# Optimization experiments

Measured on AMD Instinct MI355X. Metric: run time of the kernel, lower is better.

Reference implementation:

```python
import jax, jax.numpy as jnp
import numpy as np
from jax import lax

EPS = 1e-5
SLOPE = 0.01  # default leaky_relu negative slope

def _conv1d(x, w):
    # x: [B, Cin, L], w: [Cout, Cin, K]; padding=1 (same for K=3)
    return lax.conv_general_dilated(x, w, window_strides=(1,), padding=[(1, 1)],
                                    dimension_numbers=('NCH', 'OIH', 'NCH'))

def _bn_train(x, gamma, beta, axes):
    # training-mode BatchNorm: batch stats over `axes`, biased variance
    mean = jnp.mean(x, axis=axes, keepdims=True)
    var = jnp.mean(jnp.square(x - mean), axis=axes, keepdims=True)
    shape = [1] * x.ndim
    shape[1] = x.shape[1]
    g = gamma.reshape(shape); b = beta.reshape(shape)
    return (x - mean) * g / jnp.sqrt(var + EPS) + b

def setup_inputs() -> dict:
    key = jax.random.key(0)
    ks = jax.random.split(key, 6)
    d, d2, out_dim = 64, 128, 128
    bs, T, N = 16, 32, 256
    s = 0.05
    return {
        'x': jax.random.normal(ks[0], (bs, T, N, d), jnp.float32),
        'conv1_w': jax.random.normal(ks[1], (d2, d, 3), jnp.float32) * s,
        'bn1_g': jnp.ones((d2,), jnp.float32), 'bn1_b': jnp.zeros((d2,), jnp.float32),
        'conv2_w': jax.random.normal(ks[2], (d2, d2, 3), jnp.float32) * s,
        'bn2_g': jnp.ones((d2,), jnp.float32), 'bn2_b': jnp.zeros((d2,), jnp.float32),
        'map_w': jax.random.normal(ks[3], (d2, d2), jnp.float32) * s,
        'map_b': jnp.zeros((d2,), jnp.float32),
        'theta_w': jax.random.normal(ks[4], (out_dim, d2), jnp.float32) * s,
        'theta_b': jnp.zeros((out_dim,), jnp.float32),
        'bnS_g': jnp.ones((out_dim,), jnp.float32), 'bnS_b': jnp.zeros((out_dim,), jnp.float32),
    }

def reference(x, conv1_w, bn1_g, bn1_b, conv2_w, bn2_g, bn2_b,
              map_w, map_b, theta_w, theta_b, bnS_g, bnS_b):
    bs, T, N, d = x.shape
    d2 = 2 * d
    # ---- Temporal 1D CNN over time, per node ----
    tem = jnp.transpose(x, (0, 2, 1, 3)).reshape(bs * N, T, d)      # [BN, T, d]
    h = jnp.transpose(tem, (0, 2, 1))                               # [BN, d, T]
    h = jax.nn.relu(_bn_train(_conv1d(h, conv1_w), bn1_g, bn1_b, (0, 2)))
    h = jax.nn.relu(_bn_train(_conv1d(h, conv2_w), bn2_g, bn2_b, (0, 2)))  # [BN, 2d, T]
    # faithful raw reshape (mixes channel/time layout exactly like the torch code)
    tem_out = h.reshape(bs, N, T, d2)
    spa = jnp.transpose(tem_out, (0, 2, 1, 3)).reshape(bs * T, N, d2)  # [B', N, 2d]
    # ---- Dot-product graph construction ----
    mapped = jnp.einsum('bnd,ed->bne', spa, map_w) + map_b            # Linear(2d,2d)
    adj = jnp.einsum('bnd,bmd->bnm', mapped, mapped)                  # [B', N, N]
    eye = jnp.eye(N, dtype=adj.dtype)
    adj = jax.nn.leaky_relu(adj - eye * 1e8, SLOPE)
    adj = jax.nn.softmax(adj, axis=-1) + eye
    # ---- MPNN (k=1): theta(A @ X), BN over channels, leaky_relu ----
    agg = jnp.einsum('bnm,bmd->bnd', adj, spa)                        # bmm(A, X)
    out = jnp.einsum('bnd,od->bno', agg, theta_w) + theta_b           # [B', N, out]
    out = jnp.transpose(out, (0, 2, 1))                               # [B', out, N]
    out = _bn_train(out, bnS_g, bnS_b, (0, 2))
    out = jnp.transpose(out, (0, 2, 1))
    return jax.nn.leaky_relu(out, SLOPE)
```

## Files before the change

kernel.cpp:

```cpp
#include <hip/hip_runtime.h>

#define SLOPE 0.01f
#define EPSB 1e-5f
#define INV_CNT (1.0f/131072.0f)

typedef unsigned short u16;
typedef unsigned int u32;
typedef __attribute__((ext_vector_type(8))) short s16x8;
typedef __attribute__((ext_vector_type(4))) float f4;

__device__ float g_stats[3][2][128];
__device__ float g_sb[3][2][128];
__device__ float g_part[2048][256];
__device__ u16 g_w1h[3][128][64];
__device__ u16 g_w1l[3][128][64];
__device__ u16 g_w2h[3][128][128];
__device__ u16 g_w2l[3][128][128];
__device__ u16 g_wmh[128][128];
__device__ u16 g_wml[128][128];
__device__ u16 g_wqh[128][128];
__device__ u16 g_wql[128][128];

__device__ __forceinline__ float lrelu(float x){ return x > 0.f ? x : SLOPE*x; }
__device__ __forceinline__ u16 f2b(float f){
  u32 u = __float_as_uint(f);
  return (u16)((u + 0x7fffu + ((u >> 16) & 1u)) >> 16);
}
__device__ __forceinline__ float b2f(u16 h){ return __uint_as_float(((u32)h) << 16); }
__device__ __forceinline__ u32 pk(float a, float b){ return (u32)f2b(a) | ((u32)f2b(b) << 16); }
__device__ __forceinline__ u32 pkhl(float f){
  u16 h = f2b(f);
  u16 l = f2b(f - b2f(h));
  return (u32)h | ((u32)l << 16);
}
__device__ __forceinline__ float unhl(u32 v){ return b2f((u16)(v & 0xffff)) + b2f((u16)(v >> 16)); }

__global__ void k_zero(){
  int i = blockIdx.x*256 + threadIdx.x;
  if (i < 768) ((float*)g_stats)[i] = 0.f;
}

__global__ void k_reduce(int which){
  const float* base = &g_part[blockIdx.x*128][0];
  int j = threadIdx.x;
  float s = 0.f;
  #pragma unroll 4
  for (int r = 0; r < 128; ++r) s += base[r*256 + j];
  atomicAdd(&((float*)g_stats)[which*256 + j], s);
}

__global__ void k_prepw(const float* __restrict__ w1, const float* __restrict__ w2,
                        const float* __restrict__ mapw, const float* __restrict__ thw){
  int idx = blockIdx.x*256 + threadIdx.x;
  if (idx < 24576){
    int kk = idx >> 13, r = idx & 8191, co = r >> 6, ci = r & 63;
    float v = w1[co*192 + ci*3 + kk];
    u16 h = f2b(v);
    g_w1h[kk][co][ci] = h; g_w1l[kk][co][ci] = f2b(v - b2f(h));
  } else if (idx < 73728){
    int j = idx - 24576;
    int kk = j >> 14, r = j & 16383, co = r >> 7, ci = r & 127;
    float v = w2[co*384 + ci*3 + kk];
    u16 h = f2b(v);
    g_w2h[kk][co][ci] = h; g_w2l[kk][co][ci] = f2b(v - b2f(h));
  } else if (idx < 90112){
    int j = idx - 73728;
    float v = mapw[j];
    u16 h = f2b(v);
    ((u16*)g_wmh)[j] = h; ((u16*)g_wml)[j] = f2b(v - b2f(h));
  } else if (idx < 106496){
    int j = idx - 90112;
    float v = thw[j];
    u16 h = f2b(v);
    ((u16*)g_wqh)[j] = h; ((u16*)g_wql)[j] = f2b(v - b2f(h));
  }
}

__global__ void k_finalize(const float* __restrict__ g, const float* __restrict__ bta, int which){
  int c = threadIdx.x;
  float mean = g_stats[which][0][c] * INV_CNT;
  float var  = g_stats[which][1][c] * INV_CNT - mean*mean;
  float sc = g[c] * rsqrtf(var + EPSB);
  g_sb[which][0][c] = sc;
  g_sb[which][1][c] = bta[c] - mean*sc;
}

__global__ __launch_bounds__(256) void k_conv1(const float* __restrict__ x, u16* __restrict__ y1hl){
  __shared__ __align__(16) u16 a0h[2][34][72];
  __shared__ __align__(16) u16 a0l[2][34][72];
  __shared__ __align__(16) u16 w1s[128][72];
  const int bid = blockIdx.x;
  const int bn0 = bid*2;
  const int b = bn0 >> 8, n = bn0 & 255;
  const int tid = threadIdx.x;
  const int w = tid >> 6, l = tid & 63, quad = l >> 4, lm = l & 15;
  f4 acc[2][4];
  #pragma unroll
  for (int i = 0; i < 2; ++i)
    #pragma unroll
    for (int j = 0; j < 4; ++j) acc[i][j] = (f4)0.f;

  {
    int nn = tid >> 7, rem = tid & 127, t = rem >> 2, ci0 = (rem & 3)*16;
    const float* px = x + ((b*32 + t)*256 + n + nn)*64 + ci0;
    u16 hh[16], ll[16];
    #pragma unroll
    for (int j = 0; j < 4; ++j){
      float4 v = *(const float4*)(px + 4*j);
      float vv[4] = {v.x, v.y, v.z, v.w};
      #pragma unroll
      for (int e = 0; e < 4; ++e){
        u16 h = f2b(vv[e]);
        hh[4*j+e] = h; ll[4*j+e] = f2b(vv[e] - b2f(h));
      }
    }
    *(uint4*)&a0h[nn][t+1][ci0]   = *(uint4*)&hh[0];
    *(uint4*)&a0h[nn][t+1][ci0+8] = *(uint4*)&hh[8];
    *(uint4*)&a0l[nn][t+1][ci0]   = *(uint4*)&ll[0];
    *(uint4*)&a0l[nn][t+1][ci0+8] = *(uint4*)&ll[8];
  }
  for (int u = tid; u < 288; u += 256){
    int a = u / 144, rr = u % 144, r = rr / 36, cw = rr % 36;
    u32* base = a ? (u32*)&a0l[r>>1][(r&1)*33][0] : (u32*)&a0h[r>>1][(r&1)*33][0];
    base[cw] = 0u;
  }

  for (int kk = 0; kk < 3; ++kk){
    __syncthreads();
    { int co = tid >> 1, c0 = (tid & 1)*32;
      #pragma unroll
      for (int j = 0; j < 4; ++j)
        *(uint4*)&w1s[co][c0 + 8*j] = *(const uint4*)&g_w1h[kk][co][c0 + 8*j];
    }
    __syncthreads();
    #pragma unroll
    for (int s = 0; s < 2; ++s){
      int ci0 = s*32 + quad*8;
      s16x8 af[2], bh[4], bl[4];
      #pragma unroll
      for (int i = 0; i < 2; ++i) af[i] = *(s16x8*)&w1s[(2*w+i)*16 + lm][ci0];
      #pragma unroll
      for (int nt = 0; nt < 4; ++nt){
        bh[nt] = *(s16x8*)&a0h[nt>>1][(nt&1)*16 + lm + kk][ci0];
        bl[nt] = *(s16x8*)&a0l[nt>>1][(nt&1)*16 + lm + kk][ci0];
      }
      #pragma unroll
      for (int i = 0; i < 2; ++i)
        #pragma unroll
        for (int nt = 0; nt < 4; ++nt){
          acc[i][nt] = __builtin_amdgcn_mfma_f32_16x16x32_bf16(af[i], bh[nt], acc[i][nt], 0, 0, 0);
          acc[i][nt] = __builtin_amdgcn_mfma_f32_16x16x32_bf16(af[i], bl[nt], acc[i][nt], 0, 0, 0);
        }
    }
    __syncthreads();
    { int co = tid >> 1, c0 = (tid & 1)*32;
      #pragma unroll
      for (int j = 0; j < 4; ++j)
        *(uint4*)&w1s[co][c0 + 8*j] = *(const uint4*)&g_w1l[kk][co][c0 + 8*j];
    }
    __syncthreads();
    #pragma unroll
    for (int s = 0; s < 2; ++s){
      int ci0 = s*32 + quad*8;
      s16x8 af[2], bh[4];
      #pragma unroll
      for (int i = 0; i < 2; ++i) af[i] = *(s16x8*)&w1s[(2*w+i)*16 + lm][ci0];
      #pragma unroll
      for (int nt = 0; nt < 4; ++nt) bh[nt] = *(s16x8*)&a0h[nt>>1][(nt&1)*16 + lm + kk][ci0];
      #pragma unroll
      for (int i = 0; i < 2; ++i)
        #pragma unroll
        for (int nt = 0; nt < 4; ++nt)
          acc[i][nt] = __builtin_amdgcn_mfma_f32_16x16x32_bf16(af[i], bh[nt], acc[i][nt], 0, 0, 0);
    }
  }
  #pragma unroll
  for (int i = 0; i < 2; ++i){
    int co0 = (2*w+i)*16 + quad*4;
    float s0=0,s1=0,s2=0,s3=0,q0=0,q1=0,q2=0,q3=0;
    #pragma unroll
    for (int nt = 0; nt < 4; ++nt){
      f4 a = acc[i][nt];
      int nn = nt >> 1, t = (nt & 1)*16 + lm;
      uint4 p;
      p.x = pkhl(a.x); p.y = pkhl(a.y); p.z = pkhl(a.z); p.w = pkhl(a.w);
      *(uint4*)&y1hl[(((bn0+nn)*32 + t)*128 + co0)*2] = p;
      s0+=a.x; s1+=a.y; s2+=a.z; s3+=a.w;
      q0+=a.x*a.x; q1+=a.y*a.y; q2+=a.z*a.z; q3+=a.w*a.w;
    }
    #pragma unroll
    for (int m = 1; m < 16; m <<= 1){
      s0+=__shfl_xor(s0,m); s1+=__shfl_xor(s1,m); s2+=__shfl_xor(s2,m); s3+=__shfl_xor(s3,m);
      q0+=__shfl_xor(q0,m); q1+=__shfl_xor(q1,m); q2+=__shfl_xor(q2,m); q3+=__shfl_xor(q3,m);
    }
    if (lm == 0){
      f4 sv = {s0,s1,s2,s3}, qv = {q0,q1,q2,q3};
      *(f4*)&g_part[bid][co0]       = sv;
      *(f4*)&g_part[bid][128 + co0] = qv;
    }
  }
}

__global__ __launch_bounds__(256) void k_conv2(const u16* __restrict__ y1hl, u16* __restrict__ spa){
  __shared__ __align__(16) u16 a1s[2][34][136];
  __shared__ __align__(16) u16 w2s[128][136];
  const int bid = blockIdx.x;
  const int bn0 = bid*2;
  const int b = bn0 >> 8, n = bn0 & 255;
  const int tid = threadIdx.x;
  const int w = tid >> 6, l = tid & 63, quad = l >> 4, lm = l & 15;
  f4 acc2[4][2];
  #pragma unroll
  for (int mt = 0; mt < 4; ++mt)
    #pragma unroll
    for (int i = 0; i < 2; ++i) acc2[mt][i] = (f4)0.f;

  {
    int nn = tid >> 7, rem = tid & 127, t = rem >> 2, ci0 = (rem & 3)*32;
    const u16* py = y1hl + (((bn0+nn)*32 + t)*128)*2;
    #pragma unroll
    for (int j = 0; j < 4; ++j){
      uint4 va = *(const uint4*)&py[(ci0 + 8*j)*2];
      uint4 vb = *(const uint4*)&py[(ci0 + 8*j + 4)*2];
      u32 vv[8] = {va.x, va.y, va.z, va.w, vb.x, vb.y, vb.z, vb.w};
      u16 oo[8];
      #pragma unroll
      for (int e = 0; e < 8; ++e){
        int ci = ci0 + 8*j + e;
        float f = fmaxf(fmaf(unhl(vv[e]), g_sb[0][0][ci], g_sb[0][1][ci]), 0.f);
        oo[e] = f2b(f);
      }
      *(uint4*)&a1s[nn][t+1][ci0 + 8*j] = *(uint4*)&oo[0];
    }
  }
  for (int u = tid; u < 272; u += 256){
    int r = u/68, cw = u%68;
    ((u32*)&a1s[r>>1][(r&1)*33][0])[cw] = 0u;
  }

  for (int kk = 0; kk < 3; ++kk){
    #pragma unroll
    for (int pass = 0; pass < 2; ++pass){
      __syncthreads();
      { int co = tid >> 1, c0 = (tid & 1)*64;
        const u16* src = pass ? &g_w2l[kk][co][0] : &g_w2h[kk][co][0];
        #pragma unroll
        for (int j = 0; j < 8; ++j)
          *(uint4*)&w2s[co][c0 + 8*j] = *(const uint4*)&src[c0 + 8*j];
      }
      __syncthreads();
      #pragma unroll
      for (int s = 0; s < 4; ++s){
        int ci0 = s*32 + quad*8;
        s16x8 ax[4], bw[2];
        #pragma unroll
        for (int mt = 0; mt < 4; ++mt) ax[mt] = *(s16x8*)&a1s[mt>>1][(mt&1)*16 + lm + kk][ci0];
        #pragma unroll
        for (int i = 0; i < 2; ++i) bw[i] = *(s16x8*)&w2s[(2*w+i)*16 + lm][ci0];
        #pragma unroll
        for (int mt = 0; mt < 4; ++mt)
          #pragma unroll
          for (int i = 0; i < 2; ++i)
            acc2[mt][i] = __builtin_amdgcn_mfma_f32_16x16x32_bf16(ax[mt], bw[i], acc2[mt][i], 0, 0, 0);
      }
    }
  }
  #pragma unroll
  for (int i = 0; i < 2; ++i){
    int co = (2*w+i)*16 + lm;
    float s = 0.f, q = 0.f;
    #pragma unroll
    for (int mt = 0; mt < 4; ++mt){
      f4 a = acc2[mt][i];
      int off0 = co*32 + (mt&1)*16 + quad*4;
      int tp = off0 >> 7, cp = off0 & 127;
      int row = (b*32 + tp)*256 + (n + (mt>>1));
      uint2 p; p.x = pk(a.x, a.y); p.y = pk(a.z, a.w);
      *(uint2*)&spa[row*128 + cp] = p;
      s += a.x + a.y + a.z + a.w;
      q += a.x*a.x + a.y*a.y + a.z*a.z + a.w*a.w;
    }
    s += __shfl_xor(s, 16); s += __shfl_xor(s, 32);
    q += __shfl_xor(q, 16); q += __shfl_xor(q, 32);
    if (l < 16){
      g_part[bid][co]       = s;
      g_part[bid][128 + co] = q;
    }
  }
}

__global__ void k_act(u16* __restrict__ spa){
  int idx = blockIdx.x*256 + threadIdx.x;
  int flat = idx*8;
  int cp0 = flat & 127;
  int row = flat >> 7;
  int bpp = row >> 8;
  int tp = bpp & 31;
  int c = (tp*128 + cp0) >> 5;
  float sc = g_sb[1][0][c], bi = g_sb[1][1][c];
  uint4 v = *(uint4*)(spa + flat);
  u16 h[8]; *(uint4*)&h[0] = v;
  u16 o[8];
  #pragma unroll
  for (int i = 0; i < 8; ++i) o[i] = f2b(fmaxf(fmaf(b2f(h[i]), sc, bi), 0.f));
  *(uint4*)(spa + flat) = *(uint4*)&o[0];
}

__global__ __launch_bounds__(256) void k_gemm128b(const u16* __restrict__ A,
                                                  const float* __restrict__ bvec,
                                                  void* __restrict__ outv,
                                                  int wsel, int do_stats){
  __shared__ __align__(16) u16 As[64][136];
  __shared__ __align__(16) u16 Ws[128][136];
  const u16* Wh = wsel ? &g_wqh[0][0] : &g_wmh[0][0];
  const u16* Wl = wsel ? &g_wql[0][0] : &g_wml[0][0];
  const int bid = blockIdx.x;
  const int rowbase = bid * 64;
  const int tid = threadIdx.x;
  const int w = tid >> 6, l = tid & 63, quad = l >> 4, lm = l & 15;
  f4 acc[2][4];
  #pragma unroll
  for (int i = 0; i < 2; ++i)
    #pragma unroll
    for (int rt = 0; rt < 4; ++rt) acc[i][rt] = (f4)0.f;

  { int r = tid >> 2, c0 = (tid & 3)*32;
    #pragma unroll
    for (int j = 0; j < 4; ++j)
      *(uint4*)&As[r][c0 + 8*j] = *(const uint4*)&A[(rowbase + r)*128 + c0 + 8*j];
  }
  #pragma unroll
  for (int pass = 0; pass < 2; ++pass){
    if (pass) __syncthreads();
    { int e = tid >> 1, c0 = (tid & 1)*64;
      const u16* src = (pass ? Wl : Wh) + e*128;
      #pragma unroll
      for (int j = 0; j < 8; ++j)
        *(uint4*)&Ws[e][c0 + 8*j] = *(const uint4*)&src[c0 + 8*j];
    }
    __syncthreads();
    #pragma unroll
    for (int s = 0; s < 4; ++s){
      int k0 = s*32 + quad*8;
      s16x8 aw[2], ba[4];
      #pragma unroll
      for (int i = 0; i < 2; ++i) aw[i] = *(s16x8*)&Ws[(2*w+i)*16 + lm][k0];
      #pragma unroll
      for (int rt = 0; rt < 4; ++rt) ba[rt] = *(s16x8*)&As[rt*16 + lm][k0];
      #pragma unroll
      for (int i = 0; i < 2; ++i)
        #pragma unroll
        for (int rt = 0; rt < 4; ++rt)
          acc[i][rt] = __builtin_amdgcn_mfma_f32_16x16x32_bf16(aw[i], ba[rt], acc[i][rt], 0, 0, 0);
    }
    if (!pass) __syncthreads();
  }
  #pragma unroll
  for (int i = 0; i < 2; ++i){
    int e0 = (2*w+i)*16 + quad*4;
    f4 bv = *(const f4*)&bvec[e0];
    if (wsel == 0){
      u16* mh = (u16*)outv;
      u16* ml = mh + 16777216;
      int dc = e0 >> 5, ec = e0 & 31;
      #pragma unroll
      for (int rt = 0; rt < 4; ++rt){
        int row = rowbase + rt*16 + lm;
        int bp = row >> 8, m = row & 255;
        f4 o = acc[i][rt] + bv;
        float fv[4] = {o.x, o.y, o.z, o.w};
        u16 hh[4], ll[4];
        #pragma unroll
        for (int e = 0; e < 4; ++e){
          u16 h = f2b(fv[e]);
          hh[e] = h; ll[e] = f2b(fv[e] - b2f(h));
        }
        int off = ((bp*4 + dc)*256 + m)*32 + ec;
        *(uint2*)&mh[off] = *(uint2*)&hh[0];
        *(uint2*)&ml[off] = *(uint2*)&ll[0];
      }
    } else {
      float* outp = (float*)outv;
      f4 sv = (f4)0.f, qv = (f4)0.f;
      #pragma unroll
      for (int rt = 0; rt < 4; ++rt){
        int row = rowbase + rt*16 + lm;
        f4 o = acc[i][rt] + bv;
        *(f4*)&outp[row*128 + e0] = o;
        sv += o; qv += o*o;
      }
      if (do_stats){
        #pragma unroll
        for (int m = 1; m < 16; m <<= 1){
          sv.x+=__shfl_xor(sv.x,m); sv.y+=__shfl_xor(sv.y,m); sv.z+=__shfl_xor(sv.z,m); sv.w+=__shfl_xor(sv.w,m);
          qv.x+=__shfl_xor(qv.x,m); qv.y+=__shfl_xor(qv.y,m); qv.z+=__shfl_xor(qv.z,m); qv.w+=__shfl_xor(qv.w,m);
        }
        if (lm == 0){
          *(f4*)&g_part[bid][e0]       = sv;
          *(f4*)&g_part[bid][128 + e0] = qv;
        }
      }
    }
  }
}

__global__ __launch_bounds__(256) void k_adjagg(const u16* __restrict__ mh,
                                                const u16* __restrict__ ml,
                                                const u16* __restrict__ spa,
                                                u16* __restrict__ agg){
  __shared__ __align__(16) char smem[52224];
  u16 (*mbh)[40]   = (u16(*)[40])(smem);
  u16 (*mbl)[40]   = (u16(*)[40])(smem + 20480);
  u16 (*Ps)[264]   = (u16(*)[264])(smem);
  u16 (*spasT)[72] = (u16(*)[72])(smem + 33792);
  const int rb = blockIdx.x;
  const int vb = (rb & 7)*256 + (rb >> 3);
  const int bp = vb >> 2;
  const int nt = vb & 3;
  const int tid = threadIdx.x;
  const int w = tid >> 6, l = tid & 63, quad = l >> 4, lm = l & 15;

  f4 sacc[16];
  #pragma unroll
  for (int ct = 0; ct < 16; ++ct) sacc[ct] = (f4)0.f;

  for (int dc = 0; dc < 4; ++dc){
    __syncthreads();
    {
      const u16* srch = mh + ((bp*4 + dc) << 13);
      const u16* srcl = ml + ((bp*4 + dc) << 13);
      int m0 = tid >> 2, seg = (tid & 3)*8;
      #pragma unroll
      for (int r = 0; r < 4; ++r){
        int m = m0 + r*64;
        *(uint4*)&mbh[m][seg] = *(const uint4*)&srch[m*32 + seg];
        *(uint4*)&mbl[m][seg] = *(const uint4*)&srcl[m*32 + seg];
      }
    }
    __syncthreads();
    s16x8 amh = *(s16x8*)&mbh[nt*64 + w*16 + lm][quad*8];
    s16x8 aml = *(s16x8*)&mbl[nt*64 + w*16 + lm][quad*8];
    #pragma unroll
    for (int ct = 0; ct < 16; ++ct){
      s16x8 bmh = *(s16x8*)&mbh[ct*16 + lm][quad*8];
      s16x8 bml = *(s16x8*)&mbl[ct*16 + lm][quad*8];
      sacc[ct] = __builtin_amdgcn_mfma_f32_16x16x32_bf16(amh, bmh, sacc[ct], 0, 0, 0);
      sacc[ct] = __builtin_amdgcn_mfma_f32_16x16x32_bf16(amh, bml, sacc[ct], 0, 0, 0);
      sacc[ct] = __builtin_amdgcn_mfma_f32_16x16x32_bf16(aml, bmh, sacc[ct], 0, 0, 0);
    }
  }
  __syncthreads();

  #pragma unroll
  for (int r = 0; r < 4; ++r){
    int rowg = nt*64 + w*16 + quad*4 + r;
    float v[16]; float mx = -3.0e38f;
    #pragma unroll
    for (int ct = 0; ct < 16; ++ct){
      float t = sacc[ct][r];
      if (ct*16 + lm == rowg) t -= 1e8f;
      t = lrelu(t);
      v[ct] = t; mx = fmaxf(mx, t);
    }
    #pragma unroll
    for (int m = 1; m < 16; m <<= 1) mx = fmaxf(mx, __shfl_xor(mx, m));
    float sum = 0.f;
    #pragma unroll
    for (int ct = 0; ct < 16; ++ct){ float e = __expf(v[ct] - mx); v[ct] = e; sum += e; }
    #pragma unroll
    for (int m = 1; m < 16; m <<= 1) sum += __shfl_xor(sum, m);
    float inv = 1.0f / sum;
    #pragma unroll
    for (int ct = 0; ct < 16; ++ct)
      Ps[w*16 + quad*4 + r][ct*16 + lm] = f2b(v[ct] * inv);
  }

  f4 acc2[2][4];
  #pragma unroll
  for (int i = 0; i < 2; ++i)
    #pragma unroll
    for (int rt = 0; rt < 4; ++rt) acc2[i][rt] = (f4)0.f;

  for (int mc2 = 0; mc2 < 4; ++mc2){
    __syncthreads();
    {
      int mlo = tid & 63;
      int db = (tid >> 6)*8;
      const u16* ps = spa + (bp*256 + mc2*64 + mlo)*128;
      #pragma unroll
      for (int r = 0; r < 4; ++r){
        int d0 = db + r*32;
        uint4 v = *(const uint4*)(ps + d0);
        u16 h[8]; *(uint4*)&h[0] = v;
        #pragma unroll
        for (int j = 0; j < 8; ++j) spasT[d0+j][mlo] = h[j];
      }
    }
    __syncthreads();
    #pragma unroll
    for (int ks = 0; ks < 2; ++ks){
      int m0 = ks*32 + quad*8;
      s16x8 afs[2], bfp[4];
      #pragma unroll
      for (int i = 0; i < 2; ++i) afs[i] = *(s16x8*)&spasT[(2*w+i)*16 + lm][m0];
      #pragma unroll
      for (int rt = 0; rt < 4; ++rt) bfp[rt] = *(s16x8*)&Ps[rt*16 + lm][mc2*64 + m0];
      #pragma unroll
      for (int i = 0; i < 2; ++i)
        #pragma unroll
        for (int rt = 0; rt < 4; ++rt)
          acc2[i][rt] = __builtin_amdgcn_mfma_f32_16x16x32_bf16(afs[i], bfp[rt], acc2[i][rt], 0, 0, 0);
    }
  }
  #pragma unroll
  for (int i = 0; i < 2; ++i){
    int d0 = (2*w+i)*16 + quad*4;
    #pragma unroll
    for (int rt = 0; rt < 4; ++rt){
      int grow = bp*256 + nt*64 + rt*16 + lm;
      uint2 sp = *(const uint2*)&spa[grow*128 + d0];
      f4 a = acc2[i][rt];
      a.x += b2f((u16)(sp.x & 0xffff)); a.y += b2f((u16)(sp.x >> 16));
      a.z += b2f((u16)(sp.y & 0xffff)); a.w += b2f((u16)(sp.y >> 16));
      uint2 p; p.x = pk(a.x, a.y); p.y = pk(a.z, a.w);
      *(uint2*)&agg[grow*128 + d0] = p;
    }
  }
}

__global__ void k_bnout(float* __restrict__ outp){
  int idx = blockIdx.x*256 + threadIdx.x;
  int flat = idx*4;
  int o = flat & 127;
  float4 v = *(const float4*)(outp + flat);
  v.x = lrelu(fmaf(v.x, g_sb[2][0][o+0], g_sb[2][1][o+0]));
  v.y = lrelu(fmaf(v.y, g_sb[2][0][o+1], g_sb[2][1][o+1]));
  v.z = lrelu(fmaf(v.z, g_sb[2][0][o+2], g_sb[2][1][o+2]));
  v.w = lrelu(fmaf(v.w, g_sb[2][0][o+3], g_sb[2][1][o+3]));
  *(float4*)(outp + flat) = v;
}

extern "C" void kernel_launch(void* const* d_in, const int* in_sizes, int n_in,
                              void* d_out, int out_size, void* d_ws, size_t ws_size,
                              hipStream_t stream) {
  const float* x    = (const float*)d_in[0];
  const float* w1   = (const float*)d_in[1];
  const float* bn1g = (const float*)d_in[2];
  const float* bn1b = (const float*)d_in[3];
  const float* w2   = (const float*)d_in[4];
  const float* bn2g = (const float*)d_in[5];
  const float* bn2b = (const float*)d_in[6];
  const float* mapw = (const float*)d_in[7];
  const float* mapb = (const float*)d_in[8];
  const float* thw  = (const float*)d_in[9];
  const float* thb  = (const float*)d_in[10];
  const float* bnSg = (const float*)d_in[11];
  const float* bnSb = (const float*)d_in[12];
  float* outp = (float*)d_out;

  u16* spa = (u16*)d_ws;
  u16* agg = spa + 16777216;

  u16* y1hl = (u16*)d_out;
  u16* mh   = (u16*)d_out;
  u16* ml   = mh + 16777216;

  k_zero<<<3, 256, 0, stream>>>();
  k_prepw<<<416, 256, 0, stream>>>(w1, w2, mapw, thw);
  k_conv1<<<2048, 256, 0, stream>>>(x, y1hl);
  k_reduce<<<16, 256, 0, stream>>>(0);
  k_finalize<<<1, 128, 0, stream>>>(bn1g, bn1b, 0);
  k_conv2<<<2048, 256, 0, stream>>>(y1hl, spa);
  k_reduce<<<16, 256, 0, stream>>>(1);
  k_finalize<<<1, 128, 0, stream>>>(bn2g, bn2b, 1);
  k_act<<<8192, 256, 0, stream>>>(spa);
  k_gemm128b<<<2048, 256, 0, stream>>>(spa, mapb, (void*)mh, 0, 0);
  k_adjagg<<<2048, 256, 0, stream>>>(mh, ml, spa, agg);
  k_gemm128b<<<2048, 256, 0, stream>>>(agg, thb, (void*)outp, 1, 1);
  k_reduce<<<16, 256, 0, stream>>>(2);
  k_finalize<<<1, 128, 0, stream>>>(bnSg, bnSb, 2);
  k_bnout<<<16384, 256, 0, stream>>>(outp);
}
```

Before: 429.5 us.

## Fuse BN2+ReLU into consumers and load weights directly from global into registers

Removes the standalone k_act pass by applying the BN2 scale/bias and ReLU inline when spa is loaded in the map GEMM and in the adjacency/aggregation kernel, avoiding one full read-write of spa. The conv1, conv2 and gemm kernels no longer stage weights in shared memory. Each wave now reads its hi/lo weight fragments straight from global memory, which drops several __syncthreads and frees LDS, and launch_bounds now request 4 blocks per unit. The trade-off is redundant global and L2 weight traffic across blocks, plus recomputing the activation in two consumers.

```diff
diff --git a/kernel.cpp b/kernel.cpp
--- a/kernel.cpp
+++ b/kernel.cpp
@@ -85,10 +85,9 @@
   g_sb[which][1][c] = bta[c] - mean*sc;
 }
 
-__global__ __launch_bounds__(256) void k_conv1(const float* __restrict__ x, u16* __restrict__ y1hl){
+__global__ __launch_bounds__(256, 4) void k_conv1(const float* __restrict__ x, u16* __restrict__ y1hl){
   __shared__ __align__(16) u16 a0h[2][34][72];
   __shared__ __align__(16) u16 a0l[2][34][72];
-  __shared__ __align__(16) u16 w1s[128][72];
   const int bid = blockIdx.x;
   const int bn0 = bid*2;
   const int b = bn0 >> 8, n = bn0 & 255;
@@ -124,21 +123,18 @@
     u32* base = a ? (u32*)&a0l[r>>1][(r&1)*33][0] : (u32*)&a0h[r>>1][(r&1)*33][0];
     base[cw] = 0u;
   }
+  __syncthreads();
 
   for (int kk = 0; kk < 3; ++kk){
-    __syncthreads();
-    { int co = tid >> 1, c0 = (tid & 1)*32;
-      #pragma unroll
-      for (int j = 0; j < 4; ++j)
-        *(uint4*)&w1s[co][c0 + 8*j] = *(const uint4*)&g_w1h[kk][co][c0 + 8*j];
-    }
-    __syncthreads();
     #pragma unroll
     for (int s = 0; s < 2; ++s){
       int ci0 = s*32 + quad*8;
-      s16x8 af[2], bh[4], bl[4];
-      #pragma unroll
-      for (int i = 0; i < 2; ++i) af[i] = *(s16x8*)&w1s[(2*w+i)*16 + lm][ci0];
+      s16x8 wh[2], wl[2], bh[4], bl[4];
+      #pragma unroll
+      for (int i = 0; i < 2; ++i){
+        wh[i] = *(const s16x8*)&g_w1h[kk][(2*w+i)*16 + lm][ci0];
+        wl[i] = *(const s16x8*)&g_w1l[kk][(2*w+i)*16 + lm][ci0];
+      }
       #pragma unroll
       for (int nt = 0; nt < 4; ++nt){
         bh[nt] = *(s16x8*)&a0h[nt>>1][(nt&1)*16 + lm + kk][ci0];
@@ -148,30 +144,10 @@
       for (int i = 0; i < 2; ++i)
         #pragma unroll
         for (int nt = 0; nt < 4; ++nt){
-          acc[i][nt] = __builtin_amdgcn_mfma_f32_16x16x32_bf16(af[i], bh[nt], acc[i][nt], 0, 0, 0);
-          acc[i][nt] = __builtin_amdgcn_mfma_f32_16x16x32_bf16(af[i], bl[nt], acc[i][nt], 0, 0, 0);
+          acc[i][nt] = __builtin_amdgcn_mfma_f32_16x16x32_bf16(wh[i], bh[nt], acc[i][nt], 0, 0, 0);
+          acc[i][nt] = __builtin_amdgcn_mfma_f32_16x16x32_bf16(wh[i], bl[nt], acc[i][nt], 0, 0, 0);
+          acc[i][nt] = __builtin_amdgcn_mfma_f32_16x16x32_bf16(wl[i], bh[nt], acc[i][nt], 0, 0, 0);
         }
-    }
-    __syncthreads();
-    { int co = tid >> 1, c0 = (tid & 1)*32;
-      #pragma unroll
-      for (int j = 0; j < 4; ++j)
-        *(uint4*)&w1s[co][c0 + 8*j] = *(const uint4*)&g_w1l[kk][co][c0 + 8*j];
-    }
-    __syncthreads();
-    #pragma unroll
-    for (int s = 0; s < 2; ++s){
-      int ci0 = s*32 + quad*8;
-      s16x8 af[2], bh[4];
-      #pragma unroll
-      for (int i = 0; i < 2; ++i) af[i] = *(s16x8*)&w1s[(2*w+i)*16 + lm][ci0];
-      #pragma unroll
-      for (int nt = 0; nt < 4; ++nt) bh[nt] = *(s16x8*)&a0h[nt>>1][(nt&1)*16 + lm + kk][ci0];
-      #pragma unroll
-      for (int i = 0; i < 2; ++i)
-        #pragma unroll
-        for (int nt = 0; nt < 4; ++nt)
-          acc[i][nt] = __builtin_amdgcn_mfma_f32_16x16x32_bf16(af[i], bh[nt], acc[i][nt], 0, 0, 0);
     }
   }
   #pragma unroll
@@ -201,9 +177,8 @@
   }
 }
 
-__global__ __launch_bounds__(256) void k_conv2(const u16* __restrict__ y1hl, u16* __restrict__ spa){
+__global__ __launch_bounds__(256, 4) void k_conv2(const u16* __restrict__ y1hl, u16* __restrict__ spa){
   __shared__ __align__(16) u16 a1s[2][34][136];
-  __shared__ __align__(16) u16 w2s[128][136];
   const int bid = blockIdx.x;
   const int bn0 = bid*2;
   const int b = bn0 >> 8, n = bn0 & 255;
@@ -237,32 +212,27 @@
     int r = u/68, cw = u%68;
     ((u32*)&a1s[r>>1][(r&1)*33][0])[cw] = 0u;
   }
+  __syncthreads();
 
   for (int kk = 0; kk < 3; ++kk){
     #pragma unroll
-    for (int pass = 0; pass < 2; ++pass){
-      __syncthreads();
-      { int co = tid >> 1, c0 = (tid & 1)*64;
-        const u16* src = pass ? &g_w2l[kk][co][0] : &g_w2h[kk][co][0];
-        #pragma unroll
-        for (int j = 0; j < 8; ++j)
-          *(uint4*)&w2s[co][c0 + 8*j] = *(const uint4*)&src[c0 + 8*j];
-      }
-      __syncthreads();
-      #pragma unroll
-      for (int s = 0; s < 4; ++s){
-        int ci0 = s*32 + quad*8;
-        s16x8 ax[4], bw[2];
-        #pragma unroll
-        for (int mt = 0; mt < 4; ++mt) ax[mt] = *(s16x8*)&a1s[mt>>1][(mt&1)*16 + lm + kk][ci0];
-        #pragma unroll
-        for (int i = 0; i < 2; ++i) bw[i] = *(s16x8*)&w2s[(2*w+i)*16 + lm][ci0];
-        #pragma unroll
-        for (int mt = 0; mt < 4; ++mt)
-          #pragma unroll
-          for (int i = 0; i < 2; ++i)
-            acc2[mt][i] = __builtin_amdgcn_mfma_f32_16x16x32_bf16(ax[mt], bw[i], acc2[mt][i], 0, 0, 0);
-      }
+    for (int s = 0; s < 4; ++s){
+      int ci0 = s*32 + quad*8;
+      s16x8 ax[4], bwh[2], bwl[2];
+      #pragma unroll
+      for (int i = 0; i < 2; ++i){
+        bwh[i] = *(const s16x8*)&g_w2h[kk][(2*w+i)*16 + lm][ci0];
+        bwl[i] = *(const s16x8*)&g_w2l[kk][(2*w+i)*16 + lm][ci0];
+      }
+      #pragma unroll
+      for (int mt = 0; mt < 4; ++mt) ax[mt] = *(s16x8*)&a1s[mt>>1][(mt&1)*16 + lm + kk][ci0];
+      #pragma unroll
+      for (int mt = 0; mt < 4; ++mt)
+        #pragma unroll
+        for (int i = 0; i < 2; ++i){
+          acc2[mt][i] = __builtin_amdgcn_mfma_f32_16x16x32_bf16(ax[mt], bwh[i], acc2[mt][i], 0, 0, 0);
+          acc2[mt][i] = __builtin_amdgcn_mfma_f32_16x16x32_bf16(ax[mt], bwl[i], acc2[mt][i], 0, 0, 0);
+        }
     }
   }
   #pragma unroll
@@ -289,29 +259,11 @@
   }
 }
 
-__global__ void k_act(u16* __restrict__ spa){
-  int idx = blockIdx.x*256 + threadIdx.x;
-  int flat = idx*8;
-  int cp0 = flat & 127;
-  int row = flat >> 7;
-  int bpp = row >> 8;
-  int tp = bpp & 31;
-  int c = (tp*128 + cp0) >> 5;
-  float sc = g_sb[1][0][c], bi = g_sb[1][1][c];
-  uint4 v = *(uint4*)(spa + flat);
-  u16 h[8]; *(uint4*)&h[0] = v;
-  u16 o[8];
-  #pragma unroll
-  for (int i = 0; i < 8; ++i) o[i] = f2b(fmaxf(fmaf(b2f(h[i]), sc, bi), 0.f));
-  *(uint4*)(spa + flat) = *(uint4*)&o[0];
-}
-
-__global__ __launch_bounds__(256) void k_gemm128b(const u16* __restrict__ A,
-                                                  const float* __restrict__ bvec,
-                                                  void* __restrict__ outv,
-                                                  int wsel, int do_stats){
+__global__ __launch_bounds__(256, 4) void k_gemm128b(const u16* __restrict__ A,
+                                                     const float* __restrict__ bvec,
+                                                     void* __restrict__ outv,
+                                                     int wsel, int do_stats){
   __shared__ __align__(16) u16 As[64][136];
-  __shared__ __align__(16) u16 Ws[128][136];
   const u16* Wh = wsel ? &g_wqh[0][0] : &g_wmh[0][0];
   const u16* Wl = wsel ? &g_wql[0][0] : &g_wml[0][0];
   const int bid = blockIdx.x;
@@ -325,35 +277,48 @@
     for (int rt = 0; rt < 4; ++rt) acc[i][rt] = (f4)0.f;
 
   { int r = tid >> 2, c0 = (tid & 3)*32;
-    #pragma unroll
-    for (int j = 0; j < 4; ++j)
-      *(uint4*)&As[r][c0 + 8*j] = *(const uint4*)&A[(rowbase + r)*128 + c0 + 8*j];
-  }
-  #pragma unroll
-  for (int pass = 0; pass < 2; ++pass){
-    if (pass) __syncthreads();
-    { int e = tid >> 1, c0 = (tid & 1)*64;
-      const u16* src = (pass ? Wl : Wh) + e*128;
-      #pragma unroll
-      for (int j = 0; j < 8; ++j)
-        *(uint4*)&Ws[e][c0 + 8*j] = *(const uint4*)&src[c0 + 8*j];
-    }
-    __syncthreads();
-    #pragma unroll
-    for (int s = 0; s < 4; ++s){
-      int k0 = s*32 + quad*8;
-      s16x8 aw[2], ba[4];
-      #pragma unroll
-      for (int i = 0; i < 2; ++i) aw[i] = *(s16x8*)&Ws[(2*w+i)*16 + lm][k0];
-      #pragma unroll
-      for (int rt = 0; rt < 4; ++rt) ba[rt] = *(s16x8*)&As[rt*16 + lm][k0];
-      #pragma unroll
-      for (int i = 0; i < 2; ++i)
-        #pragma unroll
-        for (int rt = 0; rt < 4; ++rt)
-          acc[i][rt] = __builtin_amdgcn_mfma_f32_16x16x32_bf16(aw[i], ba[rt], acc[i][rt], 0, 0, 0);
-    }
-    if (!pass) __syncthreads();
+    int row = rowbase + r;
+    if (wsel == 0){
+      int c = ((row >> 8) & 31)*4 + (tid & 3);
+      float sc = g_sb[1][0][c], bi = g_sb[1][1][c];
+      #pragma unroll
+      for (int j = 0; j < 4; ++j){
+        uint4 v = *(const uint4*)&A[row*128 + c0 + 8*j];
+        u32 vv[4] = {v.x, v.y, v.z, v.w};
+        u16 oo[8];
+        #pragma unroll
+        for (int e = 0; e < 4; ++e){
+          oo[2*e]   = f2b(fmaxf(fmaf(b2f((u16)(vv[e] & 0xffff)), sc, bi), 0.f));
+          oo[2*e+1] = f2b(fmaxf(fmaf(b2f((u16)(vv[e] >> 16)),    sc, bi), 0.f));
+        }
+        *(uint4*)&As[r][c0 + 8*j] = *(uint4*)&oo[0];
+      }
+    } else {
+      #pragma unroll
+      for (int j = 0; j < 4; ++j)
+        *(uint4*)&As[r][c0 + 8*j] = *(const uint4*)&A[row*128 + c0 + 8*j];
+    }
+  }
+  __syncthreads();
+
+  #pragma unroll
+  for (int s = 0; s < 4; ++s){
+    int k0 = s*32 + quad*8;
+    s16x8 awh[2], awl[2], ba[4];
+    #pragma unroll
+    for (int i = 0; i < 2; ++i){
+      awh[i] = *(const s16x8*)&Wh[((2*w+i)*16 + lm)*128 + k0];
+      awl[i] = *(const s16x8*)&Wl[((2*w+i)*16 + lm)*128 + k0];
+    }
+    #pragma unroll
+    for (int rt = 0; rt < 4; ++rt) ba[rt] = *(s16x8*)&As[rt*16 + lm][k0];
+    #pragma unroll
+    for (int i = 0; i < 2; ++i)
+      #pragma unroll
+      for (int rt = 0; rt < 4; ++rt){
+        acc[i][rt] = __builtin_amdgcn_mfma_f32_16x16x32_bf16(awh[i], ba[rt], acc[i][rt], 0, 0, 0);
+        acc[i][rt] = __builtin_amdgcn_mfma_f32_16x16x32_bf16(awl[i], ba[rt], acc[i][rt], 0, 0, 0);
+      }
   }
   #pragma unroll
   for (int i = 0; i < 2; ++i){
@@ -419,6 +384,7 @@
   const int nt = vb & 3;
   const int tid = threadIdx.x;
   const int w = tid >> 6, l = tid & 63, quad = l >> 4, lm = l & 15;
+  const int tp4 = (bp & 31)*4;
 
   f4 sacc[16];
   #pragma unroll
@@ -490,10 +456,12 @@
       #pragma unroll
       for (int r = 0; r < 4; ++r){
         int d0 = db + r*32;
+        float sc = g_sb[1][0][tp4 + r], bi = g_sb[1][1][tp4 + r];
         uint4 v = *(const uint4*)(ps + d0);
         u16 h[8]; *(uint4*)&h[0] = v;
         #pragma unroll
-        for (int j = 0; j < 8; ++j) spasT[d0+j][mlo] = h[j];
+        for (int j = 0; j < 8; ++j)
+          spasT[d0+j][mlo] = f2b(fmaxf(fmaf(b2f(h[j]), sc, bi), 0.f));
       }
     }
     __syncthreads();
@@ -515,13 +483,17 @@
   #pragma unroll
   for (int i = 0; i < 2; ++i){
     int d0 = (2*w+i)*16 + quad*4;
+    int c = tp4 + (d0 >> 5);
+    float sc = g_sb[1][0][c], bi = g_sb[1][1][c];
     #pragma unroll
     for (int rt = 0; rt < 4; ++rt){
       int grow = bp*256 + nt*64 + rt*16 + lm;
       uint2 sp = *(const uint2*)&spa[grow*128 + d0];
       f4 a = acc2[i][rt];
-      a.x += b2f((u16)(sp.x & 0xffff)); a.y += b2f((u16)(sp.x >> 16));
-      a.z += b2f((u16)(sp.y & 0xffff)); a.w += b2f((u16)(sp.y >> 16));
+      a.x += b2f(f2b(fmaxf(fmaf(b2f((u16)(sp.x & 0xffff)), sc, bi), 0.f)));
+      a.y += b2f(f2b(fmaxf(fmaf(b2f((u16)(sp.x >> 16)),    sc, bi), 0.f)));
+      a.z += b2f(f2b(fmaxf(fmaf(b2f((u16)(sp.y & 0xffff)), sc, bi), 0.f)));
+      a.w += b2f(f2b(fmaxf(fmaf(b2f((u16)(sp.y >> 16)),    sc, bi), 0.f)));
       uint2 p; p.x = pk(a.x, a.y); p.y = pk(a.z, a.w);
       *(uint2*)&agg[grow*128 + d0] = p;
     }
@@ -573,7 +545,6 @@
   k_conv2<<<2048, 256, 0, stream>>>(y1hl, spa);
   k_reduce<<<16, 256, 0, stream>>>(1);
   k_finalize<<<1, 128, 0, stream>>>(bn2g, bn2b, 1);
-  k_act<<<8192, 256, 0, stream>>>(spa);
   k_gemm128b<<<2048, 256, 0, stream>>>(spa, mapb, (void*)mh, 0, 0);
   k_adjagg<<<2048, 256, 0, stream>>>(mh, ml, spa, agg);
   k_gemm128b<<<2048, 256, 0, stream>>>(agg, thb, (void*)outp, 1, 1);
```

Measured after the change: 406.9 us. -5.3%, faster.
